# Kernel optimization log

Hardware: AMD Instinct MI355X
Metric: run time of the kernel (lower is better)

The kernel has to match this reference:

```python
import jax, jax.numpy as jnp
import numpy as np
import math

K = 10  # k_neighbors (k = min(10, N-1) = 10 since N=2048)


def setup_inputs() -> dict:
    key = jax.random.key(0)
    k1, k2, k3, k4 = jax.random.split(key, 4)
    N, T, H = 2048, 512, 256
    E_fixed = 65536
    x = jax.random.normal(k1, (N, T, H), dtype=jnp.float32)
    fixed_edge_index = jax.random.randint(k2, (2, E_fixed), 0, N, dtype=jnp.int64)
    fixed_edge_attr = jax.random.uniform(k3, (E_fixed, 1), dtype=jnp.float32)
    W = jax.random.normal(k4, (H // 2, H), dtype=jnp.float32) / math.sqrt(H)
    mix_alpha = 0.3
    mix_logit = jnp.array([math.log(mix_alpha / (1.0 - mix_alpha + 1e-08))], dtype=jnp.float32)
    return {"x": x, "fixed_edge_index": fixed_edge_index,
            "fixed_edge_attr": fixed_edge_attr, "W": W, "mix_logit": mix_logit}


def reference(x, fixed_edge_index, fixed_edge_attr, W, mix_logit):
    # x: [N, T, H]; W: [H//2, H]; mix_logit: [1]
    N = x.shape[0]
    x_agg = x.mean(axis=1)                                  # [N, H] temporal mean-pool
    e = x_agg @ W.T                                         # [N, H//2] bias-free projection
    e = e / jnp.maximum(jnp.linalg.norm(e, axis=-1, keepdims=True), 1e-12)  # F.normalize
    sim = e @ e.T                                           # [N, N] cosine similarity
    topk_vals, topk_idx = jax.lax.top_k(sim, K + 1)         # self-sim (=1) is in column 0
    topk_vals = topk_vals[:, 1:]                            # [N, K] drop self-loop
    topk_idx = topk_idx[:, 1:]
    src = jnp.repeat(jnp.arange(N, dtype=fixed_edge_index.dtype), K)  # [N*K]
    dst = topk_idx.reshape(-1).astype(fixed_edge_index.dtype)
    dyn_edge_index = jnp.stack([src, dst], axis=0)          # [2, N*K]
    dyn_edge_attr = topk_vals.reshape(-1, 1)                # [N*K, 1]
    alpha = jax.nn.sigmoid(mix_logit[0])
    combined_edge_index = jnp.concatenate([fixed_edge_index, dyn_edge_index], axis=1)
    combined_edge_attr = jnp.concatenate(
        [fixed_edge_attr * (1.0 - alpha), dyn_edge_attr * alpha], axis=0)
    return combined_edge_index, combined_edge_attr
```

## Files before the change

### kernel.cpp

```cpp
#include <hip/hip_runtime.h>
#include <hip/hip_bf16.h>
#include <math.h>

typedef float f4 __attribute__((ext_vector_type(4)));


__global__ __launch_bounds__(256) void mean_proj_kernel(const float* __restrict__ x,
                                                        const float* __restrict__ W,
                                                        float* __restrict__ e,
                                                        int T) {
    const int n   = blockIdx.x;
    const int tid = threadIdx.x;
    const int v   = tid & 63;
    const int tg  = tid >> 6;

    __shared__ f4    red[256];
    __shared__ float xs[256];
    __shared__ float pp[256];
    __shared__ float nrm[2];

    const f4* xr = reinterpret_cast<const f4*>(x + (size_t)n * T * 256);
    f4 a0 = {0.f, 0.f, 0.f, 0.f}, a1 = a0, a2 = a0, a3 = a0;
    for (int t = tg; t < T; t += 16) {
        a0 += __builtin_nontemporal_load(&xr[(t     ) * 64 + v]);
        a1 += __builtin_nontemporal_load(&xr[(t +  4) * 64 + v]);
        a2 += __builtin_nontemporal_load(&xr[(t +  8) * 64 + v]);
        a3 += __builtin_nontemporal_load(&xr[(t + 12) * 64 + v]);
    }
    red[tid] = (a0 + a1) + (a2 + a3);
    __syncthreads();
    if (tid < 64) {
        f4 o = (red[tid] + red[tid + 64]) + (red[tid + 128] + red[tid + 192]);
        o *= (1.0f / (float)T);
        *reinterpret_cast<f4*>(&xs[tid * 4]) = o;
    }
    __syncthreads();

    {
        const int j    = tid & 127;
        const int half = tid >> 7;
        const float* Wr = W + (size_t)j * 256 + half * 128;
        const float* xh = xs + half * 128;
        float acc = 0.f;
        #pragma unroll 8
        for (int c = 0; c < 128; ++c) acc = fmaf(Wr[c], xh[c], acc);
        pp[tid] = acc;
    }
    __syncthreads();
    float accf = 0.f;
    if (tid < 128) {
        accf = pp[tid] + pp[tid + 128];
        float s = accf * accf;
        #pragma unroll
        for (int off = 32; off; off >>= 1) s += __shfl_xor(s, off);
        if ((tid & 63) == 0) nrm[tid >> 6] = s;
    }
    __syncthreads();
    if (tid < 128) {
        float inv = 1.0f / fmaxf(sqrtf(nrm[0] + nrm[1]), 1e-12f);
        e[(size_t)n * 128 + tid] = accf * inv;
    }
}

#define TK_ROWS 4
__global__ __launch_bounds__(256) void simtopk_kernel(const float* __restrict__ e,
                                                      const float* __restrict__ mix,
                                                      float* __restrict__ out,
                                                      int N , int E ) {
    __shared__ float eL[TK_ROWS][128];
    __shared__ float simL[TK_ROWS][2048];

    const int i0  = blockIdx.x * TK_ROWS;
    const int tid = threadIdx.x;
    const int M   = E + N * 10;

    {
        int r = tid >> 6;
        int c = tid & 63;
        const float* er = e + (size_t)(i0 + r) * 128;
        eL[r][c]      = er[c];
        eL[r][c + 64] = er[c + 64];
    }
    __syncthreads();

    for (int j = tid; j < N; j += 256) {
        const f4* ej = reinterpret_cast<const f4*>(e + (size_t)j * 128);
        float acc[TK_ROWS] = {0.f, 0.f, 0.f, 0.f};
        #pragma unroll 4
        for (int c4 = 0; c4 < 32; ++c4) {
            f4 vv = ej[c4];
            #pragma unroll
            for (int r = 0; r < TK_ROWS; ++r) {
                const float* el = &eL[r][c4 * 4];
                acc[r] = fmaf(vv.x, el[0], acc[r]);
                acc[r] = fmaf(vv.y, el[1], acc[r]);
                acc[r] = fmaf(vv.z, el[2], acc[r]);
                acc[r] = fmaf(vv.w, el[3], acc[r]);
            }
        }
        #pragma unroll
        for (int r = 0; r < TK_ROWS; ++r) simL[r][j] = acc[r];
    }
    __syncthreads();

    const int w    = tid >> 6;
    const int lane = tid & 63;
    const int i    = i0 + w;
    const float alpha = 1.0f / (1.0f + expf(-mix[0]));

    float keepv = 0.f;
    int   keepi = 0;
    for (int round = 0; round < 11; ++round) {
        float bv = -3.0f;
        int   bi = N;
        for (int t = 0; t < 32; ++t) {
            int j = t * 64 + lane;
            float v = simL[w][j];
            if (v > bv || (v == bv && j < bi)) { bv = v; bi = j; }
        }
        #pragma unroll
        for (int off = 32; off; off >>= 1) {
            float ov = __shfl_xor(bv, off);
            int   oi = __shfl_xor(bi, off);
            if (ov > bv || (ov == bv && oi < bi)) { bv = ov; bi = oi; }
        }
        if ((bi & 63) == lane && bi < N) simL[w][bi] = -3.0f;
        if (lane == round) { keepv = bv; keepi = bi; }
    }
    if (lane >= 1 && lane <= 10) {
        int kk  = lane - 1;
        int pos = i * 10 + kk;
        out[(size_t)E + pos]         = (float)i;
        out[(size_t)M + E + pos]     = (float)keepi;
        out[2 * (size_t)M + E + pos] = keepv * alpha;
    }
}

__global__ __launch_bounds__(256) void fixed_kernel(const int* __restrict__ ei,
                                                    const float* __restrict__ ea,
                                                    const float* __restrict__ mix,
                                                    float* __restrict__ out,
                                                    int E, int M) {
    const int idx = blockIdx.x * blockDim.x + threadIdx.x;
    if (idx < E) {
        float alpha = 1.0f / (1.0f + expf(-mix[0]));
        out[idx]                 = (float)ei[idx];
        out[(size_t)M + idx]     = (float)ei[E + idx];
        out[2 * (size_t)M + idx] = ea[idx] * (1.0f - alpha);
    }
}

extern "C" void kernel_launch(void* const* d_in, const int* in_sizes, int n_in,
                              void* d_out, int out_size, void* d_ws, size_t ws_size,
                              hipStream_t stream) {
    const float* x   = (const float*)d_in[0];
    const int*   ei  = (const int*)d_in[1];
    const float* ea  = (const float*)d_in[2];
    const float* W   = (const float*)d_in[3];
    const float* mix = (const float*)d_in[4];

    const int H  = 256;
    const int E  = in_sizes[2];
    const int M  = out_size / 3;
    const int N  = (M - E) / 10;
    const int T  = (int)((size_t)in_sizes[0] / ((size_t)N * H));

    float* e   = (float*)d_ws;
    float* out = (float*)d_out;

    mean_proj_kernel<<<N, 256, 0, stream>>>(x, W, e, T);
    simtopk_kernel<<<N / TK_ROWS, 256, 0, stream>>>(e, mix, out, N, E);
    fixed_kernel<<<(E + 255) / 256, 256, 0, stream>>>(ei, ea, mix, out, E, M);
}
```

Before: 278.3 us.

## Register-block similarity over four columns and fold fixed-edge copy into topk launch

The similarity loop now has each thread compute four columns at once, using a single vector LDS read of each query row across four candidate rows. This cuts LDS traffic per FMA and gives more independent loads in flight. The separate fixed-edge kernel is merged into the sim/top-k launch as extra trailing blocks, which removes one kernel launch. The cost is more registers per thread and a specialised N==2048 path.

```diff
diff --git a/kernel.cpp b/kernel.cpp
--- a/kernel.cpp
+++ b/kernel.cpp
@@ -64,15 +64,30 @@
 
 #define TK_ROWS 4
 __global__ __launch_bounds__(256) void simtopk_kernel(const float* __restrict__ e,
+                                                      const int* __restrict__ ei,
+                                                      const float* __restrict__ ea,
                                                       const float* __restrict__ mix,
                                                       float* __restrict__ out,
-                                                      int N , int E ) {
-    __shared__ float eL[TK_ROWS][128];
-    __shared__ float simL[TK_ROWS][2048];
-
-    const int i0  = blockIdx.x * TK_ROWS;
+                                                      int N , int E ,
+                                                      int nsimblk) {
     const int tid = threadIdx.x;
     const int M   = E + N * 10;
+    const float alpha = 1.0f / (1.0f + expf(-mix[0]));
+
+    if ((int)blockIdx.x >= nsimblk) {
+        int idx = (blockIdx.x - nsimblk) * 256 + tid;
+        if (idx < E) {
+            out[idx]                 = (float)ei[idx];
+            out[(size_t)M + idx]     = (float)ei[E + idx];
+            out[2 * (size_t)M + idx] = ea[idx] * (1.0f - alpha);
+        }
+        return;
+    }
+
+    __shared__ __align__(16) float eL[TK_ROWS][128];
+    __shared__ float simL[TK_ROWS][2048];
+
+    const int i0 = blockIdx.x * TK_ROWS;
 
     {
         int r = tid >> 6;
@@ -83,30 +98,72 @@
     }
     __syncthreads();
 
-    for (int j = tid; j < N; j += 256) {
-        const f4* ej = reinterpret_cast<const f4*>(e + (size_t)j * 128);
-        float acc[TK_ROWS] = {0.f, 0.f, 0.f, 0.f};
-        #pragma unroll 4
-        for (int c4 = 0; c4 < 32; ++c4) {
-            f4 vv = ej[c4];
+    if (N == 2048) {
+        for (int p = 0; p < 2; ++p) {
+            const int j0 = p * 1024 + tid;
+            const f4* ej = reinterpret_cast<const f4*>(e + (size_t)j0 * 128);
+            float acc[TK_ROWS][4];
             #pragma unroll
-            for (int r = 0; r < TK_ROWS; ++r) {
-                const float* el = &eL[r][c4 * 4];
-                acc[r] = fmaf(vv.x, el[0], acc[r]);
-                acc[r] = fmaf(vv.y, el[1], acc[r]);
-                acc[r] = fmaf(vv.z, el[2], acc[r]);
-                acc[r] = fmaf(vv.w, el[3], acc[r]);
+            for (int r = 0; r < TK_ROWS; ++r)
+                #pragma unroll
+                for (int q = 0; q < 4; ++q) acc[r][q] = 0.f;
+
+            for (int c4 = 0; c4 < 32; ++c4) {
+                f4 v0 = ej[c4];
+                f4 v1 = ej[c4 +  8192];
+                f4 v2 = ej[c4 + 16384];
+                f4 v3 = ej[c4 + 24576];
+                #pragma unroll
+                for (int r = 0; r < TK_ROWS; ++r) {
+                    f4 qv = *reinterpret_cast<const f4*>(&eL[r][c4 * 4]);
+                    acc[r][0] = fmaf(v0.x, qv.x, acc[r][0]);
+                    acc[r][0] = fmaf(v0.y, qv.y, acc[r][0]);
+                    acc[r][0] = fmaf(v0.z, qv.z, acc[r][0]);
+                    acc[r][0] = fmaf(v0.w, qv.w, acc[r][0]);
+                    acc[r][1] = fmaf(v1.x, qv.x, acc[r][1]);
+                    acc[r][1] = fmaf(v1.y, qv.y, acc[r][1]);
+                    acc[r][1] = fmaf(v1.z, qv.z, acc[r][1]);
+                    acc[r][1] = fmaf(v1.w, qv.w, acc[r][1]);
+                    acc[r][2] = fmaf(v2.x, qv.x, acc[r][2]);
+                    acc[r][2] = fmaf(v2.y, qv.y, acc[r][2]);
+                    acc[r][2] = fmaf(v2.z, qv.z, acc[r][2]);
+                    acc[r][2] = fmaf(v2.w, qv.w, acc[r][2]);
+                    acc[r][3] = fmaf(v3.x, qv.x, acc[r][3]);
+                    acc[r][3] = fmaf(v3.y, qv.y, acc[r][3]);
+                    acc[r][3] = fmaf(v3.z, qv.z, acc[r][3]);
+                    acc[r][3] = fmaf(v3.w, qv.w, acc[r][3]);
+                }
             }
-        }
-        #pragma unroll
-        for (int r = 0; r < TK_ROWS; ++r) simL[r][j] = acc[r];
+            #pragma unroll
+            for (int r = 0; r < TK_ROWS; ++r)
+                #pragma unroll
+                for (int q = 0; q < 4; ++q)
+                    simL[r][j0 + q * 256] = acc[r][q];
+        }
+    } else {
+        for (int j = tid; j < N; j += 256) {
+            const f4* ej = reinterpret_cast<const f4*>(e + (size_t)j * 128);
+            float acc[TK_ROWS] = {0.f, 0.f, 0.f, 0.f};
+            for (int c4 = 0; c4 < 32; ++c4) {
+                f4 vv = ej[c4];
+                #pragma unroll
+                for (int r = 0; r < TK_ROWS; ++r) {
+                    const float* el = &eL[r][c4 * 4];
+                    acc[r] = fmaf(vv.x, el[0], acc[r]);
+                    acc[r] = fmaf(vv.y, el[1], acc[r]);
+                    acc[r] = fmaf(vv.z, el[2], acc[r]);
+                    acc[r] = fmaf(vv.w, el[3], acc[r]);
+                }
+            }
+            #pragma unroll
+            for (int r = 0; r < TK_ROWS; ++r) simL[r][j] = acc[r];
+        }
     }
     __syncthreads();
 
     const int w    = tid >> 6;
     const int lane = tid & 63;
     const int i    = i0 + w;
-    const float alpha = 1.0f / (1.0f + expf(-mix[0]));
 
     float keepv = 0.f;
     int   keepi = 0;
@@ -136,20 +193,6 @@
     }
 }
 
-__global__ __launch_bounds__(256) void fixed_kernel(const int* __restrict__ ei,
-                                                    const float* __restrict__ ea,
-                                                    const float* __restrict__ mix,
-                                                    float* __restrict__ out,
-                                                    int E, int M) {
-    const int idx = blockIdx.x * blockDim.x + threadIdx.x;
-    if (idx < E) {
-        float alpha = 1.0f / (1.0f + expf(-mix[0]));
-        out[idx]                 = (float)ei[idx];
-        out[(size_t)M + idx]     = (float)ei[E + idx];
-        out[2 * (size_t)M + idx] = ea[idx] * (1.0f - alpha);
-    }
-}
-
 extern "C" void kernel_launch(void* const* d_in, const int* in_sizes, int n_in,
                               void* d_out, int out_size, void* d_ws, size_t ws_size,
                               hipStream_t stream) {
@@ -168,7 +211,9 @@
     float* e   = (float*)d_ws;
     float* out = (float*)d_out;
 
+    const int nsimblk = N / TK_ROWS;
+    const int nfixblk = (E + 255) / 256;
+
     mean_proj_kernel<<<N, 256, 0, stream>>>(x, W, e, T);
-    simtopk_kernel<<<N / TK_ROWS, 256, 0, stream>>>(e, mix, out, N, E);
-    fixed_kernel<<<(E + 255) / 256, 256, 0, stream>>>(ei, ea, mix, out, E, M);
+    simtopk_kernel<<<nsimblk + nfixblk, 256, 0, stream>>>(e, ei, ea, mix, out, N, E, nsimblk);
 }
```

New measurement: 328.9 us. +18.2%, slower.
